# Performance work log

Measured on AMD Instinct MI355X. Metric: run time of the kernel, lower is better.

The kernel has to match this reference:

```python
import jax, jax.numpy as jnp
import numpy as np

N = 40000      # nodes
E = 640000     # edges (before self-loops)
G = 64         # graphs in batch
H = 4          # heads
C = 64         # channels per head (graph_hidden_channels)
F_IN = 256     # num_node_features
NHID = 1024
NOUT = 768
NEG_SLOPE = 0.2


def setup_inputs() -> dict:
    key = jax.random.key(0)
    ks = jax.random.split(key, 20)
    s = 0.05
    inp = {
        "x": jax.random.normal(ks[0], (N, F_IN), jnp.float32),
        "edge_index": jax.random.randint(ks[1], (2, E), 0, N, dtype=jnp.int64),
        "batch": jnp.sort(jax.random.randint(ks[2], (N,), 0, G, dtype=jnp.int64)),
        # GATConv 1: in F_IN -> H heads x C
        "W1": jax.random.normal(ks[3], (F_IN, H * C), jnp.float32) * s,
        "as1": jax.random.normal(ks[4], (H, C), jnp.float32) * s,
        "ad1": jax.random.normal(ks[5], (H, C), jnp.float32) * s,
        "b1": jnp.zeros((H * C,), jnp.float32),
        # GATConv 2: in H*C -> H x C
        "W2": jax.random.normal(ks[6], (H * C, H * C), jnp.float32) * s,
        "as2": jax.random.normal(ks[7], (H, C), jnp.float32) * s,
        "ad2": jax.random.normal(ks[8], (H, C), jnp.float32) * s,
        "b2": jnp.zeros((H * C,), jnp.float32),
        # GATConv 3
        "W3": jax.random.normal(ks[9], (H * C, H * C), jnp.float32) * s,
        "as3": jax.random.normal(ks[10], (H, C), jnp.float32) * s,
        "ad3": jax.random.normal(ks[11], (H, C), jnp.float32) * s,
        "b3": jnp.zeros((H * C,), jnp.float32),
        # MLP head
        "Wm1": jax.random.normal(ks[12], (H * C, NHID), jnp.float32) * s,
        "bm1": jnp.zeros((NHID,), jnp.float32),
        "Wm2": jax.random.normal(ks[13], (NHID, NOUT), jnp.float32) * s,
        "bm2": jnp.zeros((NOUT,), jnp.float32),
    }
    return inp


def _gat_layer(x, src, dst, W, a_src, a_dst, b):
    """PyG GATConv (concat=True, self-loops already in src/dst)."""
    n = x.shape[0]
    h = (x @ W).reshape(n, H, C)                       # [N,H,C]
    # per-node attention scalars (gather scalars per edge, not full features)
    alpha_src = jnp.einsum('nhc,hc->nh', h, a_src)     # [N,H]
    alpha_dst = jnp.einsum('nhc,hc->nh', h, a_dst)     # [N,H]
    e = alpha_src[src] + alpha_dst[dst]                # [E,H]
    e = jax.nn.leaky_relu(e, NEG_SLOPE)
    # segment softmax over incoming edges of each dst node
    m = jax.ops.segment_max(e, dst, num_segments=n)    # [N,H]
    e = jnp.exp(e - m[dst])
    denom = jax.ops.segment_sum(e, dst, num_segments=n)  # [N,H]; >0 via self-loops
    alpha = e / denom[dst]                             # [E,H]
    # scatter-add weighted source features to destinations
    msg = h[src] * alpha[:, :, None]                   # [E,H,C]
    out = jax.ops.segment_sum(msg, dst, num_segments=n)  # [N,H,C]
    return out.reshape(n, H * C) + b


def reference(x, edge_index, batch,
              W1, as1, ad1, b1,
              W2, as2, ad2, b2,
              W3, as3, ad3, b3,
              Wm1, bm1, Wm2, bm2):
    n = x.shape[0]
    loops = jnp.arange(n, dtype=edge_index.dtype)
    src = jnp.concatenate([edge_index[0], loops])
    dst = jnp.concatenate([edge_index[1], loops])

    h = jax.nn.relu(_gat_layer(x, src, dst, W1, as1, ad1, b1))
    h = jax.nn.relu(_gat_layer(h, src, dst, W2, as2, ad2, b2))
    h = _gat_layer(h, src, dst, W3, as3, ad3, b3)

    # global mean pool over graphs
    sums = jax.ops.segment_sum(h, batch, num_segments=G)      # [G, H*C]
    counts = jax.ops.segment_sum(jnp.ones((n,), h.dtype), batch, num_segments=G)
    pooled = sums / jnp.maximum(counts, 1.0)[:, None]

    out = jax.nn.relu(pooled @ Wm1 + bm1)
    out = out @ Wm2 + bm2
    return out
```

## Files before the change

kernel.cpp:

```cpp
#include <hip/hip_runtime.h>
#include <hip/hip_bf16.h>
#include <math.h>

#define N_NODES 40000
#define N_EDGES 640000
#define N_GRAPH 64
#define HEADS 4
#define CHAN 64
#define HC 256
#define NHID 1024
#define NOUT 768
#define E_TOT (N_EDGES + N_NODES)
#define SCAN_NB ((N_NODES + 255) / 256)

typedef __attribute__((ext_vector_type(8))) short bf16x8;
typedef __attribute__((ext_vector_type(4))) float f32x4;

__device__ inline float bflo(unsigned u) { return __uint_as_float(u << 16); }
__device__ inline float bfhi(unsigned u) { return __uint_as_float(u & 0xffff0000u); }

__device__ inline unsigned bfbits(float f) {
    __hip_bfloat16 b = __float2bfloat16(f);
    return (unsigned)*reinterpret_cast<unsigned short*>(&b);
}
__device__ inline unsigned pk2bf(float lo, float hi) {
    return bfbits(lo) | (bfbits(hi) << 16);
}


__global__ void conv_wt3_kernel(const float* __restrict__ W1, const float* __restrict__ W2,
                                const float* __restrict__ W3, __hip_bfloat16* __restrict__ T1,
                                __hip_bfloat16* __restrict__ T2, __hip_bfloat16* __restrict__ T3) {
    const float* W = (blockIdx.y == 0) ? W1 : (blockIdx.y == 1) ? W2 : W3;
    __hip_bfloat16* T = (blockIdx.y == 0) ? T1 : (blockIdx.y == 1) ? T2 : T3;
    int k = blockIdx.x, n = threadIdx.x;
    T[(size_t)n * 256 + k] = __float2bfloat16(W[(size_t)k * 256 + n]);
}


__global__ void count_deg_kernel(const int* __restrict__ ei, int* __restrict__ deg) {
    int i = blockIdx.x * blockDim.x + threadIdx.x;
    if (i >= E_TOT) return;
    int dst = (i < N_EDGES) ? ei[N_EDGES + i] : (i - N_EDGES);
    atomicAdd(&deg[dst], 1);
}

__global__ __launch_bounds__(256)
void scan_p1_kernel(const int* __restrict__ deg, int* __restrict__ bsum) {
    const int b = blockIdx.x, t = threadIdx.x;
    const int i = b * 256 + t;
    int v = (i < N_NODES) ? deg[i] : 0;
    #pragma unroll
    for (int off = 1; off < 64; off <<= 1) v += __shfl_xor(v, off, 64);
    __shared__ int ws[4];
    if ((t & 63) == 0) ws[t >> 6] = v;
    __syncthreads();
    if (t == 0) bsum[b] = ws[0] + ws[1] + ws[2] + ws[3];
}

__global__ __launch_bounds__(256)
void scan_p2_kernel(int* __restrict__ bsum) {
    __shared__ int s[256];
    const int t = threadIdx.x;
    int v = (t < SCAN_NB) ? bsum[t] : 0;
    s[t] = v;
    __syncthreads();
    #pragma unroll
    for (int off = 1; off < 256; off <<= 1) {
        int x = (t >= off) ? s[t - off] : 0;
        __syncthreads();
        s[t] += x;
        __syncthreads();
    }
    if (t < SCAN_NB) bsum[t] = s[t] - v;
}

__global__ __launch_bounds__(256)
void scan_p3_kernel(const int* __restrict__ deg, const int* __restrict__ bsum,
                    int* __restrict__ rowptr) {
    __shared__ int s[256];
    const int b = blockIdx.x, t = threadIdx.x;
    const int i = b * 256 + t;
    int v = (i < N_NODES) ? deg[i] : 0;
    s[t] = v;
    __syncthreads();
    #pragma unroll
    for (int off = 1; off < 256; off <<= 1) {
        int x = (t >= off) ? s[t - off] : 0;
        __syncthreads();
        s[t] += x;
        __syncthreads();
    }
    if (i < N_NODES) rowptr[i] = bsum[b] + s[t] - v;
    if (i == 0) rowptr[N_NODES] = E_TOT;
}

__global__ void fill_csr_kernel(const int* __restrict__ ei, const int* __restrict__ rowptr,
                                int* __restrict__ cursor, int* __restrict__ csr_src) {
    int i = blockIdx.x * blockDim.x + threadIdx.x;
    if (i >= E_TOT) return;
    int src, dst;
    if (i < N_EDGES) { src = ei[i]; dst = ei[N_EDGES + i]; }
    else             { src = dst = i - N_EDGES; }
    int pos = atomicAdd(&cursor[dst], 1);
    csr_src[rowptr[dst] + pos] = src;
}


template<int CAST>
__global__ __launch_bounds__(512, 2)
void gemm_mfma_kernel(const void* __restrict__ Ain, const __hip_bfloat16* __restrict__ Wt,
                      __hip_bfloat16* __restrict__ C,
                      const float* __restrict__ a_s, const float* __restrict__ a_d,
                      float* __restrict__ asrc, float* __restrict__ adst) {
    __shared__ ushort Wl[128 * 256];

    const int tid = threadIdx.x;
    const int lane = tid & 63;
    const int l15 = lane & 15, lq = lane >> 4;
    const int w = tid >> 6;
    const int hsel = w >> 2;
    const int stripe = w & 3;
    const int head = blockIdx.y * 2 + hsel;
    const int row_base = blockIdx.x * 320;

    {
        const int col = tid >> 2;
        const char* Wb = (const char*)(Wt + (size_t)(blockIdx.y * 128 + col) * 256);
        #pragma unroll
        for (int j = 0; j < 8; j++) {
            int q = (tid & 3) * 8 + j;
            uint4 v = *reinterpret_cast<const uint4*>(Wb + q * 16);
            *reinterpret_cast<uint4*>(&Wl[col * 256 + ((q ^ (col & 7)) * 8)]) = v;
        }
    }
    __syncthreads();

    bf16x8 b[8][4];
    #pragma unroll
    for (int kt = 0; kt < 8; kt++)
        #pragma unroll
        for (int n = 0; n < 4; n++) {
            int cl = hsel * 64 + n * 16 + l15;
            int q = kt * 4 + lq;
            b[kt][n] = *reinterpret_cast<const bf16x8*>(&Wl[cl * 256 + ((q ^ (cl & 7)) * 8)]);
        }

    float was[4], wad[4];
    #pragma unroll
    for (int n = 0; n < 4; n++) {
        was[n] = a_s[head * 64 + n * 16 + l15];
        wad[n] = a_d[head * 64 + n * 16 + l15];
    }

    auto loadA = [&](int T, bf16x8* a) {
        const int row = row_base + T * 16 + l15;
        if (CAST) {
            const float* Af = (const float*)Ain;
            #pragma unroll
            for (int kt = 0; kt < 8; kt++) {
                float4 u0 = *reinterpret_cast<const float4*>(&Af[(size_t)row * 256 + kt * 32 + lq * 8]);
                float4 u1 = *reinterpret_cast<const float4*>(&Af[(size_t)row * 256 + kt * 32 + lq * 8 + 4]);
                uint4 uv = make_uint4(pk2bf(u0.x, u0.y), pk2bf(u0.z, u0.w),
                                      pk2bf(u1.x, u1.y), pk2bf(u1.z, u1.w));
                a[kt] = *reinterpret_cast<bf16x8*>(&uv);
            }
        } else {
            const __hip_bfloat16* Ab = (const __hip_bfloat16*)Ain;
            #pragma unroll
            for (int kt = 0; kt < 8; kt++) {
                uint4 uv = *reinterpret_cast<const uint4*>(&Ab[(size_t)row * 256 + kt * 32 + lq * 8]);
                a[kt] = *reinterpret_cast<bf16x8*>(&uv);
            }
        }
    };

    bf16x8 aA[8], aB[8];
    loadA(stripe, aA);
    #pragma unroll
    for (int ti = 0; ti < 5; ti++) {
        const int T = stripe + ti * 4;
        if (ti < 4) loadA(T + 4, aB);
        f32x4 acc[4];
        #pragma unroll
        for (int n = 0; n < 4; n++) acc[n] = (f32x4){0.f, 0.f, 0.f, 0.f};
        #pragma unroll
        for (int kt = 0; kt < 8; kt++)
            #pragma unroll
            for (int n = 0; n < 4; n++)
                acc[n] = __builtin_amdgcn_mfma_f32_16x16x32_bf16(aA[kt], b[kt][n], acc[n], 0, 0, 0);

        #pragma unroll
        for (int reg = 0; reg < 4; reg++) {
            float ps = 0.f, pd = 0.f;
            #pragma unroll
            for (int n = 0; n < 4; n++) {
                float v = acc[n][reg];
                ps = fmaf(v, was[n], ps);
                pd = fmaf(v, wad[n], pd);
            }
            #pragma unroll
            for (int off = 1; off < 16; off <<= 1) {
                ps += __shfl_xor(ps, off, 16);
                pd += __shfl_xor(pd, off, 16);
            }
            const int row = row_base + T * 16 + lq * 4 + reg;
            if (l15 == 0) {
                asrc[row * 4 + head] = ps;
                adst[row * 4 + head] = pd;
            }
        }
        #pragma unroll
        for (int n = 0; n < 4; n++)
            #pragma unroll
            for (int reg = 0; reg < 4; reg++) {
                float v = acc[n][reg];
                float vp = __shfl_xor(v, 1, 16);
                const int row = row_base + T * 16 + lq * 4 + reg;
                if (!(l15 & 1)) {
                    unsigned pk = pk2bf(v, vp);
                    *reinterpret_cast<unsigned*>(&C[(size_t)row * 256 + head * 64 + n * 16 + l15]) = pk;
                }
            }
        #pragma unroll
        for (int kk = 0; kk < 8; kk++) aA[kk] = aB[kk];
    }
}


#define ACHUNK 256

__global__ __launch_bounds__(256)
void gat_fused_agg(const __hip_bfloat16* __restrict__ h, const float* __restrict__ asrc,
                   const float* __restrict__ adst, const int* __restrict__ rowptr,
                   const int* __restrict__ csr_src, const float* __restrict__ bias,
                   __hip_bfloat16* __restrict__ out, int do_relu) {
    __shared__ int   s_src[ACHUNK];
    __shared__ float s_w[ACHUNK][5];
    __shared__ float s_acc[8][HC];
    __shared__ float s_sum[4];

    const int n = blockIdx.x;
    const int t = threadIdx.x;
    const int lane = t & 63;
    const int wid = t >> 6;
    const int grp = t >> 5;
    const int gl  = t & 31;
    const int h3  = gl >> 3;
    const int start = rowptr[n];
    const int deg = rowptr[n + 1] - start;
    const float ad = adst[n * 4 + wid];

    float ssum = 0.f;
    float acc[8] = {0.f, 0.f, 0.f, 0.f, 0.f, 0.f, 0.f, 0.f};

    for (int c0 = 0; c0 < deg; c0 += ACHUNK) {
        const int cn = min(ACHUNK, deg - c0);
        if (c0) __syncthreads();
        for (int e = lane; e < cn; e += 64) {
            int src = csr_src[start + c0 + e];
            if (wid == 0) s_src[e] = src;
            float sc = asrc[src * 4 + wid] + ad;
            sc = (sc >= 0.f) ? sc : 0.2f * sc;
            float w = __expf(sc);
            s_w[e][wid] = w;
            ssum += w;
        }
        __syncthreads();
        #pragma unroll 2
        for (int e = grp; e < cn; e += 8) {
            float w = s_w[e][h3];
            uint4 v = *reinterpret_cast<const uint4*>(&h[(size_t)s_src[e] * HC + gl * 8]);
            acc[0] = fmaf(w, bflo(v.x), acc[0]);
            acc[1] = fmaf(w, bfhi(v.x), acc[1]);
            acc[2] = fmaf(w, bflo(v.y), acc[2]);
            acc[3] = fmaf(w, bfhi(v.y), acc[3]);
            acc[4] = fmaf(w, bflo(v.z), acc[4]);
            acc[5] = fmaf(w, bfhi(v.z), acc[5]);
            acc[6] = fmaf(w, bflo(v.w), acc[6]);
            acc[7] = fmaf(w, bfhi(v.w), acc[7]);
        }
    }
    #pragma unroll
    for (int off = 1; off < 64; off <<= 1) ssum += __shfl_xor(ssum, off, 64);
    if (lane == 0) s_sum[wid] = ssum;
    *reinterpret_cast<float4*>(&s_acc[grp][gl * 8])     = make_float4(acc[0], acc[1], acc[2], acc[3]);
    *reinterpret_cast<float4*>(&s_acc[grp][gl * 8 + 4]) = make_float4(acc[4], acc[5], acc[6], acc[7]);
    __syncthreads();
    float tot = 0.f;
    #pragma unroll
    for (int g = 0; g < 8; g++) tot += s_acc[g][t];
    float r = tot / s_sum[t >> 6] + bias[t];
    if (do_relu) r = fmaxf(r, 0.f);
    out[(size_t)n * HC + t] = __float2bfloat16(r);
}


__global__ __launch_bounds__(1024)
void pool_mlp1_kernel(const __hip_bfloat16* __restrict__ h, const int* __restrict__ batch,
                      const float* __restrict__ Wm1, const float* __restrict__ bm1,
                      float* __restrict__ hidden) {
    __shared__ float s_part[4][256];
    __shared__ float row[256];
    const int g = blockIdx.x, t = threadIdx.x;
    int lo = 0, hi = N_NODES;
    while (lo < hi) { int mid = (lo + hi) >> 1; if (batch[mid] < g) lo = mid + 1; else hi = mid; }
    const int start = lo;
    lo = 0; hi = N_NODES;
    while (lo < hi) { int mid = (lo + hi) >> 1; if (batch[mid] < g + 1) lo = mid + 1; else hi = mid; }
    const int end = lo;

    const int sub = t >> 8, ch = t & 255;
    float a = 0.f;
    for (int n = start + sub; n < end; n += 4)
        a += __bfloat162float(h[(size_t)n * HC + ch]);
    s_part[sub][ch] = a;
    __syncthreads();
    if (t < 256) {
        float c = (float)max(end - start, 1);
        row[t] = (s_part[0][t] + s_part[1][t] + s_part[2][t] + s_part[3][t]) / c;
    }
    __syncthreads();
    float acc = bm1[t];
    for (int k = 0; k < 256; k++) acc = fmaf(row[k], Wm1[(size_t)k * NHID + t], acc);
    hidden[(size_t)g * NHID + t] = fmaxf(acc, 0.f);
}

__global__ __launch_bounds__(768)
void mlp2_kernel(const float* __restrict__ hidden, const float* __restrict__ W,
                 const float* __restrict__ b, float* __restrict__ out) {
    __shared__ float row[NHID];
    const int g = blockIdx.x, t = threadIdx.x;
    row[t] = hidden[g * NHID + t];
    if (t < NHID - NOUT) row[NOUT + t] = hidden[g * NHID + NOUT + t];
    __syncthreads();
    float acc = b[t];
    for (int k = 0; k < NHID; k++) acc = fmaf(row[k], W[(size_t)k * NOUT + t], acc);
    out[g * NOUT + t] = acc;
}


extern "C" void kernel_launch(void* const* d_in, const int* in_sizes, int n_in,
                              void* d_out, int out_size, void* d_ws, size_t ws_size,
                              hipStream_t stream) {
    const float* x  = (const float*)d_in[0];
    const int* ei   = (const int*)d_in[1];
    const int* batch = (const int*)d_in[2];
    const float* W1 = (const float*)d_in[3];
    const float* as1 = (const float*)d_in[4];
    const float* ad1 = (const float*)d_in[5];
    const float* b1 = (const float*)d_in[6];
    const float* W2 = (const float*)d_in[7];
    const float* as2 = (const float*)d_in[8];
    const float* ad2 = (const float*)d_in[9];
    const float* b2 = (const float*)d_in[10];
    const float* W3 = (const float*)d_in[11];
    const float* as3 = (const float*)d_in[12];
    const float* ad3 = (const float*)d_in[13];
    const float* b3 = (const float*)d_in[14];
    const float* Wm1 = (const float*)d_in[15];
    const float* bm1 = (const float*)d_in[16];
    const float* Wm2 = (const float*)d_in[17];
    const float* bm2 = (const float*)d_in[18];
    float* out = (float*)d_out;

    char* base = (char*)d_ws;
    size_t off = 0;
    auto alloc = [&](size_t bytes) { char* p = base + off; off = (off + bytes + 255) & ~(size_t)255; return p; };
    __hip_bfloat16* hA   = (__hip_bfloat16*)alloc((size_t)N_NODES * 256 * 2);
    __hip_bfloat16* hB   = (__hip_bfloat16*)alloc((size_t)N_NODES * 256 * 2);
    __hip_bfloat16* Wt1  = (__hip_bfloat16*)alloc((size_t)256 * 256 * 2);
    __hip_bfloat16* Wt2  = (__hip_bfloat16*)alloc((size_t)256 * 256 * 2);
    __hip_bfloat16* Wt3  = (__hip_bfloat16*)alloc((size_t)256 * 256 * 2);
    float* asrc   = (float*)alloc((size_t)N_NODES * 4 * 4);
    float* adst   = (float*)alloc((size_t)N_NODES * 4 * 4);
    int*   deg    = (int*)alloc((size_t)N_NODES * 4);
    int*   cursor = (int*)alloc((size_t)N_NODES * 4);
    int*   rowptr = (int*)alloc((size_t)(N_NODES + 1) * 4);
    int*   bsum   = (int*)alloc((size_t)SCAN_NB * 4);
    int*   csrsrc = (int*)alloc((size_t)E_TOT * 4);
    float* hidden = (float*)alloc((size_t)N_GRAPH * NHID * 4);
    (void)ws_size; (void)n_in; (void)in_sizes; (void)out_size;

    hipMemsetAsync(deg, 0, (size_t)N_NODES * 4 * 2, stream);

    conv_wt3_kernel<<<dim3(256, 3), 256, 0, stream>>>(W1, W2, W3, Wt1, Wt2, Wt3);

    const int eb = (E_TOT + 255) / 256;
    count_deg_kernel<<<eb, 256, 0, stream>>>(ei, deg);
    scan_p1_kernel<<<SCAN_NB, 256, 0, stream>>>(deg, bsum);
    scan_p2_kernel<<<1, 256, 0, stream>>>(bsum);
    scan_p3_kernel<<<SCAN_NB, 256, 0, stream>>>(deg, bsum, rowptr);
    fill_csr_kernel<<<eb, 256, 0, stream>>>(ei, rowptr, cursor, csrsrc);

    const dim3 ggrid(125, 2);

    gemm_mfma_kernel<1><<<ggrid, 512, 0, stream>>>(x, Wt1, hA, as1, ad1, asrc, adst);
    gat_fused_agg<<<N_NODES, 256, 0, stream>>>(hA, asrc, adst, rowptr, csrsrc, b1, hB, 1);
    gemm_mfma_kernel<0><<<ggrid, 512, 0, stream>>>(hB, Wt2, hA, as2, ad2, asrc, adst);
    gat_fused_agg<<<N_NODES, 256, 0, stream>>>(hA, asrc, adst, rowptr, csrsrc, b2, hB, 1);
    gemm_mfma_kernel<0><<<ggrid, 512, 0, stream>>>(hB, Wt3, hA, as3, ad3, asrc, adst);
    gat_fused_agg<<<N_NODES, 256, 0, stream>>>(hA, asrc, adst, rowptr, csrsrc, b3, hB, 0);

    pool_mlp1_kernel<<<N_GRAPH, 1024, 0, stream>>>(hB, batch, Wm1, bm1, hidden);
    mlp2_kernel<<<N_GRAPH, NOUT, 0, stream>>>(hidden, Wm2, bm2, out);
}
```

Before: 431.6 us.

## Split pooling from MLP and tile MLP GEMMs across graphs

Pooling now runs in its own kernel, reading 16-byte bf16 vectors with 8 row groups per block. The two MLP layers become shared-memory tiled GEMMs: each block computes a 64-column slice for all 64 graphs. Before, each graph's block re-read the full weight matrix, so Wm1 and Wm2 were streamed 64 times. The change adds one kernel launch and the small grids (16 and 12 blocks) leave most of the GPU idle.

Result: slower. 557.9 us (+29.3%).

```diff
diff --git a/kernel.cpp b/kernel.cpp
--- a/kernel.cpp
+++ b/kernel.cpp
@@ -296,13 +296,14 @@
 }
 
 
-__global__ __launch_bounds__(1024)
-void pool_mlp1_kernel(const __hip_bfloat16* __restrict__ h, const int* __restrict__ batch,
-                      const float* __restrict__ Wm1, const float* __restrict__ bm1,
-                      float* __restrict__ hidden) {
-    __shared__ float s_part[4][256];
-    __shared__ float row[256];
-    const int g = blockIdx.x, t = threadIdx.x;
+__global__ __launch_bounds__(256)
+void pool_kernel(const __hip_bfloat16* __restrict__ h, const int* __restrict__ batch,
+                 float* __restrict__ pooled_mean) {
+    __shared__ float s_acc[8][HC];
+    const int g = blockIdx.x;
+    const int t = threadIdx.x;
+    const int grp = t >> 5;
+    const int gl  = t & 31;
     int lo = 0, hi = N_NODES;
     while (lo < hi) { int mid = (lo + hi) >> 1; if (batch[mid] < g) lo = mid + 1; else hi = mid; }
     const int start = lo;
@@ -310,33 +311,99 @@
     while (lo < hi) { int mid = (lo + hi) >> 1; if (batch[mid] < g + 1) lo = mid + 1; else hi = mid; }
     const int end = lo;
 
-    const int sub = t >> 8, ch = t & 255;
-    float a = 0.f;
-    for (int n = start + sub; n < end; n += 4)
-        a += __bfloat162float(h[(size_t)n * HC + ch]);
-    s_part[sub][ch] = a;
-    __syncthreads();
-    if (t < 256) {
-        float c = (float)max(end - start, 1);
-        row[t] = (s_part[0][t] + s_part[1][t] + s_part[2][t] + s_part[3][t]) / c;
-    }
-    __syncthreads();
-    float acc = bm1[t];
-    for (int k = 0; k < 256; k++) acc = fmaf(row[k], Wm1[(size_t)k * NHID + t], acc);
-    hidden[(size_t)g * NHID + t] = fmaxf(acc, 0.f);
-}
-
-__global__ __launch_bounds__(768)
-void mlp2_kernel(const float* __restrict__ hidden, const float* __restrict__ W,
-                 const float* __restrict__ b, float* __restrict__ out) {
-    __shared__ float row[NHID];
-    const int g = blockIdx.x, t = threadIdx.x;
-    row[t] = hidden[g * NHID + t];
-    if (t < NHID - NOUT) row[NOUT + t] = hidden[g * NHID + NOUT + t];
-    __syncthreads();
-    float acc = b[t];
-    for (int k = 0; k < NHID; k++) acc = fmaf(row[k], W[(size_t)k * NOUT + t], acc);
-    out[g * NOUT + t] = acc;
+    float acc[8] = {0.f, 0.f, 0.f, 0.f, 0.f, 0.f, 0.f, 0.f};
+    for (int n = start + grp; n < end; n += 8) {
+        uint4 v = *reinterpret_cast<const uint4*>(&h[(size_t)n * HC + gl * 8]);
+        acc[0] += bflo(v.x); acc[1] += bfhi(v.x);
+        acc[2] += bflo(v.y); acc[3] += bfhi(v.y);
+        acc[4] += bflo(v.z); acc[5] += bfhi(v.z);
+        acc[6] += bflo(v.w); acc[7] += bfhi(v.w);
+    }
+    #pragma unroll
+    for (int j = 0; j < 8; j++) s_acc[grp][gl * 8 + j] = acc[j];
+    __syncthreads();
+    float tot = 0.f;
+    #pragma unroll
+    for (int q = 0; q < 8; q++) tot += s_acc[q][t];
+    const float inv = 1.0f / (float)max(end - start, 1);
+    pooled_mean[g * HC + t] = tot * inv;
+}
+
+
+__global__ __launch_bounds__(256)
+void mlp1_tiled(const float* __restrict__ pm, const float* __restrict__ Wm1,
+                const float* __restrict__ bm1, float* __restrict__ hidden) {
+    __shared__ float Ps[64][65];
+    __shared__ float Ws[64][65];
+    const int t = threadIdx.x;
+    const int colb = blockIdx.x * 64;
+    const int col = t & 63;
+    const int g0 = (t >> 6) * 16;
+    float acc[16];
+    #pragma unroll
+    for (int i = 0; i < 16; i++) acc[i] = 0.f;
+
+    for (int kc = 0; kc < 4; kc++) {
+        if (kc) __syncthreads();
+        #pragma unroll
+        for (int j = 0; j < 16; j++) {
+            int e = t + j * 256;
+            int gg = e >> 6, kk = e & 63;
+            Ps[gg][kk] = pm[gg * HC + kc * 64 + kk];
+            Ws[gg][kk] = Wm1[(size_t)(kc * 64 + gg) * NHID + colb + kk];
+        }
+        __syncthreads();
+        #pragma unroll 8
+        for (int k = 0; k < 64; k++) {
+            float wv = Ws[k][col];
+            #pragma unroll
+            for (int i = 0; i < 16; i++)
+                acc[i] = fmaf(Ps[g0 + i][k], wv, acc[i]);
+        }
+    }
+    float bv = bm1[colb + col];
+    #pragma unroll
+    for (int i = 0; i < 16; i++)
+        hidden[(size_t)(g0 + i) * NHID + colb + col] = fmaxf(acc[i] + bv, 0.f);
+}
+
+
+__global__ __launch_bounds__(256)
+void mlp2_tiled(const float* __restrict__ hidden, const float* __restrict__ Wm2,
+                const float* __restrict__ bm2, float* __restrict__ out) {
+    __shared__ float Hs[64][129];
+    __shared__ float Ws[128][65];
+    const int t = threadIdx.x;
+    const int colb = blockIdx.x * 64;
+    const int col = t & 63;
+    const int g0 = (t >> 6) * 16;
+    float acc[16];
+    #pragma unroll
+    for (int i = 0; i < 16; i++) acc[i] = 0.f;
+
+    for (int kc = 0; kc < 8; kc++) {
+        if (kc) __syncthreads();
+        #pragma unroll
+        for (int j = 0; j < 32; j++) {
+            int e = t + j * 256;
+            int gg = e >> 7, kk = e & 127;
+            Hs[gg][kk] = hidden[(size_t)gg * NHID + kc * 128 + kk];
+            int k2 = e >> 6, c2 = e & 63;
+            Ws[k2][c2] = Wm2[(size_t)(kc * 128 + k2) * NOUT + colb + c2];
+        }
+        __syncthreads();
+        #pragma unroll 8
+        for (int k = 0; k < 128; k++) {
+            float wv = Ws[k][col];
+            #pragma unroll
+            for (int i = 0; i < 16; i++)
+                acc[i] = fmaf(Hs[g0 + i][k], wv, acc[i]);
+        }
+    }
+    float bv = bm2[colb + col];
+    #pragma unroll
+    for (int i = 0; i < 16; i++)
+        out[(size_t)(g0 + i) * NOUT + colb + col] = acc[i] + bv;
 }
 
 
@@ -379,6 +446,7 @@
     int*   rowptr = (int*)alloc((size_t)(N_NODES + 1) * 4);
     int*   bsum   = (int*)alloc((size_t)SCAN_NB * 4);
     int*   csrsrc = (int*)alloc((size_t)E_TOT * 4);
+    float* pmean  = (float*)alloc((size_t)N_GRAPH * 256 * 4);
     float* hidden = (float*)alloc((size_t)N_GRAPH * NHID * 4);
     (void)ws_size; (void)n_in; (void)in_sizes; (void)out_size;
 
@@ -402,6 +470,7 @@
     gemm_mfma_kernel<0><<<ggrid, 512, 0, stream>>>(hB, Wt3, hA, as3, ad3, asrc, adst);
     gat_fused_agg<<<N_NODES, 256, 0, stream>>>(hA, asrc, adst, rowptr, csrsrc, b3, hB, 0);
 
-    pool_mlp1_kernel<<<N_GRAPH, 1024, 0, stream>>>(hB, batch, Wm1, bm1, hidden);
-    mlp2_kernel<<<N_GRAPH, NOUT, 0, stream>>>(hidden, Wm2, bm2, out);
-}
+    pool_kernel<<<N_GRAPH, 256, 0, stream>>>(hB, batch, pmean);
+    mlp1_tiled<<<NHID / 64, 256, 0, stream>>>(pmean, Wm1, bm1, hidden);
+    mlp2_tiled<<<NOUT / 64, 256, 0, stream>>>(hidden, Wm2, bm2, out);
+}
```

## Stage GEMM output through LDS for wide stores; split-K the final MLP

Applied to the files above, without the earlier changes.

The GEMM epilogue now writes each wave's fp32 accumulator tile into a padded LDS strip that reuses the weight buffer. It then reads the strip back row-wise, so each lane packs 16 bf16 values and issues two 16-byte global stores, replacing many 4-byte scattered stores. The second MLP layer is split over 8 K-chunks across a 64x8 grid, with a separate reduction kernel adding bias. This raises parallelism beyond 64 blocks at the cost of an extra launch and a partial buffer. An added barrier protects reuse of the weight LDS region.

After: 410.3 us. 4.9% less time.

```diff
diff --git a/kernel.cpp b/kernel.cpp
--- a/kernel.cpp
+++ b/kernel.cpp
@@ -145,6 +145,9 @@
             int q = kt * 4 + lq;
             b[kt][n] = *reinterpret_cast<const bf16x8*>(&Wl[cl * 256 + ((q ^ (cl & 7)) * 8)]);
         }
+    __syncthreads();
+
+    float* strip = reinterpret_cast<float*>(Wl) + w * (16 * 68);
 
     float was[4], wad[4];
     #pragma unroll
@@ -213,15 +216,24 @@
         #pragma unroll
         for (int n = 0; n < 4; n++)
             #pragma unroll
-            for (int reg = 0; reg < 4; reg++) {
-                float v = acc[n][reg];
-                float vp = __shfl_xor(v, 1, 16);
-                const int row = row_base + T * 16 + lq * 4 + reg;
-                if (!(l15 & 1)) {
-                    unsigned pk = pk2bf(v, vp);
-                    *reinterpret_cast<unsigned*>(&C[(size_t)row * 256 + head * 64 + n * 16 + l15]) = pk;
-                }
-            }
+            for (int reg = 0; reg < 4; reg++)
+                strip[(lq * 4 + reg) * 68 + n * 16 + l15] = acc[n][reg];
+        {
+            const int r  = lane >> 2;
+            const int cq = lane & 3;
+            f32x4 c0 = *reinterpret_cast<const f32x4*>(&strip[r * 68 + cq * 16]);
+            f32x4 c1 = *reinterpret_cast<const f32x4*>(&strip[r * 68 + cq * 16 + 4]);
+            f32x4 c2 = *reinterpret_cast<const f32x4*>(&strip[r * 68 + cq * 16 + 8]);
+            f32x4 c3 = *reinterpret_cast<const f32x4*>(&strip[r * 68 + cq * 16 + 12]);
+            uint4 o0 = make_uint4(pk2bf(c0[0], c0[1]), pk2bf(c0[2], c0[3]),
+                                  pk2bf(c1[0], c1[1]), pk2bf(c1[2], c1[3]));
+            uint4 o1 = make_uint4(pk2bf(c2[0], c2[1]), pk2bf(c2[2], c2[3]),
+                                  pk2bf(c3[0], c3[1]), pk2bf(c3[2], c3[3]));
+            const int row = row_base + T * 16 + r;
+            __hip_bfloat16* Cp = C + (size_t)row * 256 + head * 64 + cq * 16;
+            *reinterpret_cast<uint4*>(Cp) = o0;
+            *reinterpret_cast<uint4*>(Cp + 8) = o1;
+        }
         #pragma unroll
         for (int kk = 0; kk < 8; kk++) aA[kk] = aB[kk];
     }
@@ -326,17 +338,30 @@
     hidden[(size_t)g * NHID + t] = fmaxf(acc, 0.f);
 }
 
+
 __global__ __launch_bounds__(768)
-void mlp2_kernel(const float* __restrict__ hidden, const float* __restrict__ W,
-                 const float* __restrict__ b, float* __restrict__ out) {
-    __shared__ float row[NHID];
+void mlp2_partial(const float* __restrict__ hidden, const float* __restrict__ W,
+                  float* __restrict__ partial) {
+    __shared__ float row[128];
+    const int g = blockIdx.x, ks = blockIdx.y, t = threadIdx.x;
+    if (t < 128) row[t] = hidden[(size_t)g * NHID + ks * 128 + t];
+    __syncthreads();
+    float acc = 0.f;
+    const float* Wp = W + (size_t)(ks * 128) * NOUT + t;
+    #pragma unroll 4
+    for (int k = 0; k < 128; k++) acc = fmaf(row[k], Wp[(size_t)k * NOUT], acc);
+    partial[((size_t)ks * N_GRAPH + g) * NOUT + t] = acc;
+}
+
+__global__ __launch_bounds__(768)
+void mlp2_reduce(const float* __restrict__ partial, const float* __restrict__ b,
+                 float* __restrict__ out) {
     const int g = blockIdx.x, t = threadIdx.x;
-    row[t] = hidden[g * NHID + t];
-    if (t < NHID - NOUT) row[NOUT + t] = hidden[g * NHID + NOUT + t];
-    __syncthreads();
     float acc = b[t];
-    for (int k = 0; k < NHID; k++) acc = fmaf(row[k], W[(size_t)k * NOUT + t], acc);
-    out[g * NOUT + t] = acc;
+    #pragma unroll
+    for (int ks = 0; ks < 8; ks++)
+        acc += partial[((size_t)ks * N_GRAPH + g) * NOUT + t];
+    out[(size_t)g * NOUT + t] = acc;
 }
 
 
@@ -380,6 +405,7 @@
     int*   bsum   = (int*)alloc((size_t)SCAN_NB * 4);
     int*   csrsrc = (int*)alloc((size_t)E_TOT * 4);
     float* hidden = (float*)alloc((size_t)N_GRAPH * NHID * 4);
+    float* part2  = (float*)alloc((size_t)8 * N_GRAPH * NOUT * 4);
     (void)ws_size; (void)n_in; (void)in_sizes; (void)out_size;
 
     hipMemsetAsync(deg, 0, (size_t)N_NODES * 4 * 2, stream);
@@ -403,5 +429,6 @@
     gat_fused_agg<<<N_NODES, 256, 0, stream>>>(hA, asrc, adst, rowptr, csrsrc, b3, hB, 0);
 
     pool_mlp1_kernel<<<N_GRAPH, 1024, 0, stream>>>(hB, batch, Wm1, bm1, hidden);
-    mlp2_kernel<<<N_GRAPH, NOUT, 0, stream>>>(hidden, Wm2, bm2, out);
-}
+    mlp2_partial<<<dim3(N_GRAPH, 8), 768, 0, stream>>>(hidden, Wm2, part2);
+    mlp2_reduce<<<N_GRAPH, 768, 0, stream>>>(part2, bm2, out);
+}
```
